# Kernel tuning notes

Hardware: AMD Instinct MI355X
Metric: run time of the kernel (lower is better)

The kernel has to match this reference:

```python
import jax, jax.numpy as jnp
import numpy as np

K_CLS, M_PROTO, C = 19, 10, 720
EPS_SK, SK_ITERS = 0.05, 3  # standard distributed_sinkhorn defaults (SwAV/ProtoSeg)


def _layernorm(x, g, b, eps=1e-5):
    mu = jnp.mean(x, axis=-1, keepdims=True)
    var = jnp.var(x, axis=-1, keepdims=True)
    return (x - mu) * jax.lax.rsqrt(var + eps) * g + b


def _l2n(x):
    return x / jnp.clip(jnp.linalg.norm(x, axis=-1, keepdims=True), 1e-12, None)


def _masked_sinkhorn(scores, mask):
    # scores: [K, N, M] per-class similarity; mask: [K, N] (1.0 where gt_seg == class k)
    # Faithful to distributed_sinkhorn(init_q) run per class, vectorized over classes
    # with masking instead of data-dependent boolean gather (jit-safe).
    L = jnp.exp(scores / EPS_SK) * mask[..., None]                     # [K, N, M]
    L = L / jnp.clip(jnp.sum(L, axis=(1, 2), keepdims=True), 1e-12, None)
    n = jnp.sum(mask, axis=1)[:, None, None]                           # pixels per class [K,1,1]
    n_safe = jnp.maximum(n, 1.0)

    def body(L, _):
        # normalize each prototype row (sum over pixels), then divide by M
        L = L / jnp.clip(jnp.sum(L, axis=1, keepdims=True), 1e-12, None) / M_PROTO
        # normalize each pixel column (sum over prototypes), then divide by n
        L = L / jnp.clip(jnp.sum(L, axis=2, keepdims=True), 1e-12, None) / n_safe
        L = L * mask[..., None]
        return L, None

    L, _ = jax.lax.scan(body, L, None, length=SK_ITERS)
    return L * n_safe                                                  # [K, N, M]


def setup_inputs() -> dict:
    key = jax.random.key(0)
    k1, k2, k3 = jax.random.split(key, 3)
    N = 4 * 128 * 128  # batch 4, 512x512 crop at HRNet output stride 4
    return {
        "x": jax.random.normal(k1, (N, C), jnp.float32),
        "gt_seg": jax.random.randint(k2, (N,), 0, K_CLS),
        "feat_gamma": jnp.ones((C,), jnp.float32),
        "feat_beta": jnp.zeros((C,), jnp.float32),
        "prototypes": jax.random.normal(k3, (K_CLS, M_PROTO, C), jnp.float32) * 0.02,
    }


def reference(x, gt_seg, feat_gamma, feat_beta, prototypes):
    # similarity_compute (cosine branch)
    xn = _l2n(_layernorm(x, feat_gamma, feat_beta))                    # [N, C]
    protos = _l2n(prototypes)                                          # [K, M, C]
    sim_mat = jnp.einsum('nd,kmd->nmk', xn, protos)                    # [N, M, K]

    # prototype_learning
    s = jnp.max(sim_mat, axis=1)                                       # amax over prototypes -> [N, K]
    pred_seg = jnp.argmax(s, axis=-1)                                  # [N]
    scores = jnp.transpose(sim_mat, (2, 0, 1))                         # [K, N, M]
    mask = jnp.transpose(jax.nn.one_hot(gt_seg, K_CLS, dtype=sim_mat.dtype))  # [K, N]
    q = _masked_sinkhorn(scores, mask)                                 # [K, N, M]
    return sim_mat, q, pred_seg
```

## Files before the change

### kernel.cpp

```cpp
#include <hip/hip_runtime.h>
#include <stdint.h>

#define N_PIX    65536
#define C_DIM    720
#define K_CLS    19
#define M_PROTO  10
#define NPROTO   190
#define CPAD     768
#define OFF_Q    12451840
#define OFF_PRED 24903680

typedef _Float16 half8 __attribute__((ext_vector_type(8)));
typedef float    f32x4 __attribute__((ext_vector_type(4)));

#define WS_E       0u
#define WS_G2      768u
#define WS_G3      1536u
#define WS_CNT     2304u
#define WS_TIECNT  2432u
#define WS_V       2560u
#define WS_PSCALE  4096u
#define WS_EPIX    1052672u
#define WS_U       3674112u
#define WS_TIELIST 3936256u
#define WS_PF16    4198400u
#define WS_PF32    4493312u

__global__ void zero_acc(float* ws) {
    if (threadIdx.x < 640) ws[threadIdx.x] = 0.f;
}

__global__ void proto_prep(const float* __restrict__ protos,
                           _Float16* __restrict__ pf16,
                           float* __restrict__ pf32) {
    int p = blockIdx.x;
    int tid = threadIdx.x;
    if (p >= NPROTO) {
        for (int c = tid; c < CPAD; c += 256) pf16[(size_t)p * CPAD + c] = (_Float16)0.f;
        return;
    }
    __shared__ float red[256];
    const float* row = protos + (size_t)p * C_DIM;
    float ss = 0.f;
    for (int c = tid; c < C_DIM; c += 256) { float v = row[c]; ss += v * v; }
    red[tid] = ss;
    __syncthreads();
    for (int s = 128; s > 0; s >>= 1) {
        if (tid < s) red[tid] += red[tid + s];
        __syncthreads();
    }
    float invn = 1.f / fmaxf(sqrtf(red[0]), 1e-12f);
    for (int c = tid; c < CPAD; c += 256) {
        float v = (c < C_DIM) ? row[c] * invn : 0.f;
        pf16[(size_t)p * CPAD + c] = (_Float16)v;
        if (c < C_DIM) pf32[(size_t)p * C_DIM + c] = v;
    }
}

__global__ void stats_kernel(const float* __restrict__ x,
                             const float* __restrict__ gamma,
                             const float* __restrict__ beta,
                             float4* __restrict__ pscale) {
    int wave = threadIdx.x >> 6, lane = threadIdx.x & 63;
    int n = blockIdx.x * 4 + wave;
    const float* row = x + (size_t)n * C_DIM;
    float a[8];
    #pragma unroll
    for (int t = 0; t < 8; ++t) a[t] = 0.f;
    #pragma unroll
    for (int j = 0; j < 12; ++j) {
        int i = lane + 64 * j;
        if (i < C_DIM) {
            float v = row[i], g = gamma[i], b = beta[i];
            float g2 = g * g;
            a[0] += v;          a[1] += v * v;
            a[2] += v * g2;     a[3] += v * v * g2;
            a[4] += v * g * b;  a[5] += g2;
            a[6] += g * b;      a[7] += b * b;
        }
    }
    #pragma unroll
    for (int m = 1; m < 64; m <<= 1) {
        #pragma unroll
        for (int t = 0; t < 8; ++t) a[t] += __shfl_xor(a[t], m);
    }
    if (lane == 0) {
        float mu   = a[0] * (1.f / 720.f);
        float var  = a[1] * (1.f / 720.f) - mu * mu;
        float rsig = rsqrtf(var + 1e-5f);
        float ny2  = rsig * rsig * (a[3] - 2.f * mu * a[2] + mu * mu * a[5])
                   + 2.f * rsig * (a[4] - mu * a[6]) + a[7];
        float rn   = 1.f / fmaxf(sqrtf(fmaxf(ny2, 0.f)), 1e-12f);
        float pp   = rsig * rn;
        pscale[n]  = make_float4(pp, -pp * mu, rn, 0.f);
    }
}

__global__ __launch_bounds__(256) void gemm_sim(
        const float*  __restrict__ x,
        const float4* __restrict__ pscale,
        const float*  __restrict__ gamma,
        const float*  __restrict__ beta,
        const _Float16* __restrict__ pf16,
        float* __restrict__ out) {
    __shared__ __align__(16) char smem[36864];
    _Float16* xs = (_Float16*)smem;
    _Float16* ps = (_Float16*)(smem + 9216);

    int tid = threadIdx.x;
    int wave = tid >> 6, lane = tid & 63;
    int lane15 = lane & 15, quad = lane >> 4;
    int n0 = blockIdx.x * 64;

    f32x4 acc[12];
    #pragma unroll
    for (int ct = 0; ct < 12; ++ct)
        acc[ct] = (f32x4){0.f, 0.f, 0.f, 0.f};

    #pragma unroll 1
    for (int ch = 0; ch < 12; ++ch) {
        __syncthreads();
        int kb4 = ch * 16;
        #pragma unroll
        for (int i = 0; i < 4; ++i) {
            int idx = tid + 256 * i;
            int r = idx >> 4, c4 = idx & 15;
            int gc4 = kb4 + c4;
            float4 xv = make_float4(0.f, 0.f, 0.f, 0.f);
            float4 gv = xv, bv = xv;
            if (gc4 < 180) {
                xv = *(const float4*)(x + (size_t)(n0 + r) * C_DIM + gc4 * 4);
                gv = *(const float4*)(gamma + gc4 * 4);
                bv = *(const float4*)(beta + gc4 * 4);
            }
            float4 sc = pscale[n0 + r];
            union { _Float16 h[4]; uint2 u; } cv;
            cv.h[0] = (_Float16)((sc.x * xv.x + sc.y) * gv.x + sc.z * bv.x);
            cv.h[1] = (_Float16)((sc.x * xv.y + sc.y) * gv.y + sc.z * bv.y);
            cv.h[2] = (_Float16)((sc.x * xv.z + sc.y) * gv.z + sc.z * bv.z);
            cv.h[3] = (_Float16)((sc.x * xv.w + sc.y) * gv.w + sc.z * bv.w);
            *reinterpret_cast<uint2*>(&xs[r * 72 + c4 * 4]) = cv.u;
        }
        #pragma unroll
        for (int i = 0; i < 6; ++i) {
            int idx = tid + 256 * i;
            int r = idx >> 3, c8 = idx & 7;
            int4 v = *(const int4*)(pf16 + (size_t)r * CPAD + ch * 64 + c8 * 8);
            *reinterpret_cast<int4*>(&ps[r * 72 + c8 * 8]) = v;
        }
        __syncthreads();
        #pragma unroll
        for (int ks = 0; ks < 2; ++ks) {
            int col = ks * 32 + quad * 8;
            half8 a0 = *reinterpret_cast<const half8*>(&xs[(wave * 16 + lane15) * 72 + col]);
            half8 b[12];
            #pragma unroll
            for (int ct = 0; ct < 12; ++ct)
                b[ct] = *reinterpret_cast<const half8*>(&ps[(ct * 16 + lane15) * 72 + col]);
            #pragma unroll
            for (int ct = 0; ct < 12; ++ct)
                acc[ct] = __builtin_amdgcn_mfma_f32_16x16x32_f16(a0, b[ct], acc[ct], 0, 0, 0);
        }
    }

    __syncthreads();
    float* ebuf = (float*)smem + wave * 1600;
    #pragma unroll
    for (int h = 0; h < 2; ++h) {
        if ((quad >> 1) == h) {
            int prow = (quad - 2 * h) * 4;
            #pragma unroll
            for (int ct = 0; ct < 12; ++ct) {
                int proto = ct * 16 + lane15;
                if (proto < NPROTO) {
                    int kc = proto / 10;
                    int m = proto - kc * 10;
                    int obase = m * 19 + kc;
                    #pragma unroll
                    for (int r = 0; r < 4; ++r)
                        ebuf[(prow + r) * 200 + obase] = acc[ct][r];
                }
            }
        }
        __syncthreads();
        #pragma unroll
        for (int p = 0; p < 8; ++p) {
            int pixel = n0 + wave * 16 + 8 * h + p;
            #pragma unroll
            for (int j = 0; j < 3; ++j) {
                int col = lane + 64 * j;
                if (col < NPROTO)
                    out[(size_t)pixel * 190 + col] = ebuf[p * 200 + col];
            }
        }
        __syncthreads();
    }
}

__global__ void reduce_pred(const float* __restrict__ sim,
                            const int* __restrict__ gt_seg,
                            float* __restrict__ out_pred,
                            float* __restrict__ epix,
                            float* __restrict__ E,
                            float* __restrict__ cnt,
                            int* __restrict__ tiecnt,
                            int* __restrict__ tielist) {
    __shared__ float Ek[192];
    __shared__ float hist[20];
    int tid = threadIdx.x;
    if (tid < 192) Ek[tid] = 0.f;
    if (tid < 20) hist[tid] = 0.f;
    __syncthreads();
    int n = blockIdx.x * 256 + tid;
    const float* row = sim + (size_t)n * 190;
    const float2* rp2 = reinterpret_cast<const float2*>(row);
    float s[19];
    #pragma unroll
    for (int k = 0; k < 19; ++k) s[k] = -1e30f;
    #pragma unroll
    for (int i = 0; i < 95; ++i) {
        float2 d = rp2[i];
        s[(2 * i) % 19]     = fmaxf(s[(2 * i) % 19], d.x);
        s[(2 * i + 1) % 19] = fmaxf(s[(2 * i + 1) % 19], d.y);
    }
    float best = s[0], second = -1e30f;
    int bk = 0;
    #pragma unroll
    for (int k = 1; k < 19; ++k) {
        float v = s[k];
        if (v > best) { second = best; best = v; bk = k; }
        else if (v > second) second = v;
    }
    out_pred[n] = (float)bk;
    if (best - second < 3e-4f) {
        int pos = atomicAdd(tiecnt, 1);
        if (pos < N_PIX) tielist[pos] = n;
    }
    int g = gt_seg[n];
    #pragma unroll
    for (int m = 0; m < 10; ++m) {
        float ev = __expf(row[m * 19 + g] * 20.f);
        epix[(size_t)n * 10 + m] = ev;
        atomicAdd(&Ek[g * 10 + m], ev);
    }
    atomicAdd(&hist[g], 1.f);
    __syncthreads();
    if (tid < 190) atomicAdd(&E[tid], Ek[tid]);
    if (tid < 19) atomicAdd(&cnt[tid], hist[tid]);
}

__global__ void tiefix(const float* __restrict__ x,
                       const float4* __restrict__ pscale,
                       const float* __restrict__ gamma,
                       const float* __restrict__ beta,
                       const float* __restrict__ pf32,
                       const int* __restrict__ tiecnt,
                       const int* __restrict__ tielist,
                       float* __restrict__ out_pred) {
    __shared__ float xrow[720];
    __shared__ double sd[190];
    int count = *tiecnt;
    if (count > N_PIX) count = N_PIX;
    int wave = threadIdx.x >> 6, lane = threadIdx.x & 63;
    for (int it = blockIdx.x; it < count; it += gridDim.x) {
        int n = tielist[it];
        float4 sc = pscale[n];
        for (int c = threadIdx.x; c < 720; c += 256)
            xrow[c] = (sc.x * x[(size_t)n * 720 + c] + sc.y) * gamma[c] + sc.z * beta[c];
        __syncthreads();
        for (int p = wave; p < NPROTO; p += 4) {
            const float* pr = pf32 + (size_t)p * 720;
            double a = 0.0;
            for (int j = 0; j < 12; ++j) {
                int i = lane + 64 * j;
                if (i < 720) a += (double)xrow[i] * (double)pr[i];
            }
            #pragma unroll
            for (int m = 1; m < 64; m <<= 1) a += __shfl_xor(a, m);
            if (lane == 0) sd[p] = a;
        }
        __syncthreads();
        if (threadIdx.x == 0) {
            double best = -1e300;
            int bk = 0;
            for (int k = 0; k < 19; ++k) {
                double sk = -1e300;
                for (int m = 0; m < 10; ++m) sk = fmax(sk, sd[k * 10 + m]);
                if (sk > best) { best = sk; bk = k; }
            }
            out_pred[n] = (float)bk;
        }
        __syncthreads();
    }
}

__global__ void v1k(const float* __restrict__ E, float* __restrict__ v) {
    __shared__ float Es[192];
    int t = threadIdx.x;
    if (t < 192) Es[t] = (t < 190) ? E[t] : 0.f;
    __syncthreads();
    if (t < 190) {
        int k = t / 10;
        float S = 0.f;
        #pragma unroll
        for (int m = 0; m < 10; ++m) S += Es[k * 10 + m];
        float v0 = 1.f / fmaxf(S, 1e-12f);
        float r = v0 * Es[t];
        v[t] = v0 / (fmaxf(r, 1e-12f) * 10.f);
    }
}

__global__ void v23k(float* __restrict__ v, const float* __restrict__ G) {
    int t = threadIdx.x;
    if (t < 190) {
        float r = v[t] * G[t];
        v[t] = v[t] / (fmaxf(r, 1e-12f) * 10.f);
    }
}

__global__ void pk(const float* __restrict__ epix,
                   const int* __restrict__ gt_seg,
                   const float* __restrict__ v,
                   const float* __restrict__ cnt,
                   const float* __restrict__ uin,
                   float* __restrict__ uout,
                   float* __restrict__ G) {
    __shared__ float vs[190];
    __shared__ float cs[19];
    __shared__ float Ga[190];
    int tid = threadIdx.x;
    if (tid < 190) { vs[tid] = v[tid]; Ga[tid] = 0.f; }
    if (tid < 19) cs[tid] = cnt[tid];
    __syncthreads();
    int n = blockIdx.x * 256 + tid;
    int g = gt_seg[n];
    float ns = fmaxf(cs[g], 1.f);
    const float* e = epix + (size_t)n * 10;
    float ev[10];
    float dot = 0.f;
    #pragma unroll
    for (int m = 0; m < 10; ++m) { ev[m] = e[m]; dot += ev[m] * vs[g * 10 + m]; }
    float up = uin ? uin[n] : 1.f;
    float c = up * dot;
    float u = up / (fmaxf(c, 1e-12f) * ns);
    uout[n] = u;
    #pragma unroll
    for (int m = 0; m < 10; ++m) atomicAdd(&Ga[g * 10 + m], ev[m] * u);
    __syncthreads();
    if (tid < 190) atomicAdd(&G[tid], Ga[tid]);
}

__global__ void p3k(const float* __restrict__ epix,
                    const int* __restrict__ gt_seg,
                    const float* __restrict__ v,
                    const float* __restrict__ cnt,
                    const float* __restrict__ uin,
                    float* __restrict__ qout) {
    __shared__ float vs[190];
    __shared__ float cs[19];
    int tid = threadIdx.x;
    if (tid < 190) vs[tid] = v[tid];
    if (tid < 19) cs[tid] = cnt[tid];
    __syncthreads();
    int n = blockIdx.x * 256 + tid;
    int g = gt_seg[n];
    float ns = fmaxf(cs[g], 1.f);
    const float* e = epix + (size_t)n * 10;
    float ev[10];
    float dot = 0.f;
    #pragma unroll
    for (int m = 0; m < 10; ++m) { ev[m] = e[m]; dot += ev[m] * vs[g * 10 + m]; }
    float up = uin[n];
    float c = up * dot;
    float u3 = up / (fmaxf(c, 1e-12f) * ns);
    float2 qv[5];
    #pragma unroll
    for (int j = 0; j < 5; ++j) {
        qv[j].x = ev[2 * j] * u3 * vs[g * 10 + 2 * j] * ns;
        qv[j].y = ev[2 * j + 1] * u3 * vs[g * 10 + 2 * j + 1] * ns;
    }
    const float2 z2 = make_float2(0.f, 0.f);
    for (int k = 0; k < 19; ++k) {
        float2* dst = reinterpret_cast<float2*>(qout + (size_t)k * 655360 + (size_t)n * 10);
        if (k == g) {
            #pragma unroll
            for (int j = 0; j < 5; ++j) dst[j] = qv[j];
        } else {
            #pragma unroll
            for (int j = 0; j < 5; ++j) dst[j] = z2;
        }
    }
}

extern "C" void kernel_launch(void* const* d_in, const int* in_sizes, int n_in,
                              void* d_out, int out_size, void* d_ws, size_t ws_size,
                              hipStream_t stream) {
    const float* x      = (const float*)d_in[0];
    const int*   gt     = (const int*)d_in[1];
    const float* gamma  = (const float*)d_in[2];
    const float* beta   = (const float*)d_in[3];
    const float* protos = (const float*)d_in[4];
    float* out = (float*)d_out;
    char* ws = (char*)d_ws;

    float*  E       = (float*)(ws + WS_E);
    float*  G2      = (float*)(ws + WS_G2);
    float*  G3      = (float*)(ws + WS_G3);
    float*  cnt     = (float*)(ws + WS_CNT);
    int*    tiecnt  = (int*)(ws + WS_TIECNT);
    float*  v       = (float*)(ws + WS_V);
    float4* pscale  = (float4*)(ws + WS_PSCALE);
    float*  epix    = (float*)(ws + WS_EPIX);
    float*  u       = (float*)(ws + WS_U);
    int*    tielist = (int*)(ws + WS_TIELIST);
    _Float16* pf16  = (_Float16*)(ws + WS_PF16);
    float*  pf32    = (float*)(ws + WS_PF32);

    zero_acc<<<1, 1024, 0, stream>>>((float*)ws);
    proto_prep<<<192, 256, 0, stream>>>(protos, pf16, pf32);
    stats_kernel<<<16384, 256, 0, stream>>>(x, gamma, beta, pscale);
    gemm_sim<<<1024, 256, 0, stream>>>(x, pscale, gamma, beta, pf16, out);
    reduce_pred<<<256, 256, 0, stream>>>(out, gt, out + OFF_PRED, epix, E, cnt, tiecnt, tielist);
    tiefix<<<1024, 256, 0, stream>>>(x, pscale, gamma, beta, pf32, tiecnt, tielist, out + OFF_PRED);
    v1k<<<1, 256, 0, stream>>>(E, v);
    pk<<<256, 256, 0, stream>>>(epix, gt, v, cnt, nullptr, u, G2);
    v23k<<<1, 256, 0, stream>>>(v, G2);
    pk<<<256, 256, 0, stream>>>(epix, gt, v, cnt, u, u, G3);
    v23k<<<1, 256, 0, stream>>>(v, G3);
    p3k<<<256, 256, 0, stream>>>(epix, gt, v, cnt, u, out + OFF_Q);
}
```

Before: 523.7 us.

## Fuse argmax, tie detection and exp/class sums into GEMM epilogue

Removes the separate reduce_pred kernel and computes per-pixel class maxima, argmax, tie listing, exp scores and per-class accumulations inside the gemm_sim epilogue from the LDS staging buffer. This avoids re-reading the 50MB similarity matrix from global memory and saves a launch. The trade-off is a longer epilogue that runs only 8 lanes per wave for the argmax and exp part, and extra barriers.

Measured after the change: 496.4 us. 5.2% less time.

```diff
diff --git a/kernel.cpp b/kernel.cpp
--- a/kernel.cpp
+++ b/kernel.cpp
@@ -102,7 +102,14 @@
         const float*  __restrict__ gamma,
         const float*  __restrict__ beta,
         const _Float16* __restrict__ pf16,
-        float* __restrict__ out) {
+        const int*    __restrict__ gt_seg,
+        float* __restrict__ out_sim,
+        float* __restrict__ out_pred,
+        float* __restrict__ epix,
+        float* __restrict__ E,
+        float* __restrict__ cnt,
+        int*   __restrict__ tiecnt,
+        int*   __restrict__ tielist) {
     __shared__ __align__(16) char smem[36864];
     _Float16* xs = (_Float16*)smem;
     _Float16* ps = (_Float16*)(smem + 9216);
@@ -164,7 +171,14 @@
     }
 
     __syncthreads();
-    float* ebuf = (float*)smem + wave * 1600;
+    float* fsm   = (float*)smem;
+    float* ebuf  = fsm + wave * 1600;
+    float* smaxw = fsm + 6400 + wave * 152;
+    float* Eks   = fsm + 7008;
+    float* hists = fsm + 7200;
+    if (tid < 212) fsm[7008 + tid] = 0.f;
+    __syncthreads();
+
     #pragma unroll
     for (int h = 0; h < 2; ++h) {
         if ((quad >> 1) == h) {
@@ -190,63 +204,49 @@
             for (int j = 0; j < 3; ++j) {
                 int col = lane + 64 * j;
                 if (col < NPROTO)
-                    out[(size_t)pixel * 190 + col] = ebuf[p * 200 + col];
-            }
-        }
-        __syncthreads();
-    }
-}
-
-__global__ void reduce_pred(const float* __restrict__ sim,
-                            const int* __restrict__ gt_seg,
-                            float* __restrict__ out_pred,
-                            float* __restrict__ epix,
-                            float* __restrict__ E,
-                            float* __restrict__ cnt,
-                            int* __restrict__ tiecnt,
-                            int* __restrict__ tielist) {
-    __shared__ float Ek[192];
-    __shared__ float hist[20];
-    int tid = threadIdx.x;
-    if (tid < 192) Ek[tid] = 0.f;
-    if (tid < 20) hist[tid] = 0.f;
-    __syncthreads();
-    int n = blockIdx.x * 256 + tid;
-    const float* row = sim + (size_t)n * 190;
-    const float2* rp2 = reinterpret_cast<const float2*>(row);
-    float s[19];
-    #pragma unroll
-    for (int k = 0; k < 19; ++k) s[k] = -1e30f;
-    #pragma unroll
-    for (int i = 0; i < 95; ++i) {
-        float2 d = rp2[i];
-        s[(2 * i) % 19]     = fmaxf(s[(2 * i) % 19], d.x);
-        s[(2 * i + 1) % 19] = fmaxf(s[(2 * i + 1) % 19], d.y);
-    }
-    float best = s[0], second = -1e30f;
-    int bk = 0;
-    #pragma unroll
-    for (int k = 1; k < 19; ++k) {
-        float v = s[k];
-        if (v > best) { second = best; best = v; bk = k; }
-        else if (v > second) second = v;
-    }
-    out_pred[n] = (float)bk;
-    if (best - second < 3e-4f) {
-        int pos = atomicAdd(tiecnt, 1);
-        if (pos < N_PIX) tielist[pos] = n;
-    }
-    int g = gt_seg[n];
-    #pragma unroll
-    for (int m = 0; m < 10; ++m) {
-        float ev = __expf(row[m * 19 + g] * 20.f);
-        epix[(size_t)n * 10 + m] = ev;
-        atomicAdd(&Ek[g * 10 + m], ev);
-    }
-    atomicAdd(&hist[g], 1.f);
-    __syncthreads();
-    if (tid < 190) atomicAdd(&E[tid], Ek[tid]);
-    if (tid < 19) atomicAdd(&cnt[tid], hist[tid]);
+                    out_sim[(size_t)pixel * 190 + col] = ebuf[p * 200 + col];
+            }
+        }
+        #pragma unroll
+        for (int t = lane; t < 152; t += 64) {
+            int p = t / 19, k = t - p * 19;
+            const float* row = ebuf + p * 200;
+            float mx = row[k];
+            #pragma unroll
+            for (int m = 1; m < 10; ++m) mx = fmaxf(mx, row[m * 19 + k]);
+            smaxw[t] = mx;
+        }
+        __syncthreads();
+        if (lane < 8) {
+            int p = lane;
+            int pixel = n0 + wave * 16 + 8 * h + p;
+            float best = smaxw[p * 19], second = -1e30f;
+            int bk = 0;
+            #pragma unroll
+            for (int k = 1; k < 19; ++k) {
+                float v = smaxw[p * 19 + k];
+                if (v > best) { second = best; best = v; bk = k; }
+                else if (v > second) second = v;
+            }
+            out_pred[pixel] = (float)bk;
+            if (best - second < 3e-4f) {
+                int pos = atomicAdd(tiecnt, 1);
+                if (pos < N_PIX) tielist[pos] = pixel;
+            }
+            int g = gt_seg[pixel];
+            atomicAdd(&hists[g], 1.f);
+            const float* row = ebuf + p * 200;
+            #pragma unroll
+            for (int m = 0; m < 10; ++m) {
+                float ev = __expf(row[m * 19 + g] * 20.f);
+                epix[(size_t)pixel * 10 + m] = ev;
+                atomicAdd(&Eks[g * 10 + m], ev);
+            }
+        }
+        __syncthreads();
+    }
+    if (tid < 190) atomicAdd(&E[tid], Eks[tid]);
+    if (tid < 19)  atomicAdd(&cnt[tid], hists[tid]);
 }
 
 __global__ void tiefix(const float* __restrict__ x,
@@ -419,8 +419,8 @@
     zero_acc<<<1, 1024, 0, stream>>>((float*)ws);
     proto_prep<<<192, 256, 0, stream>>>(protos, pf16, pf32);
     stats_kernel<<<16384, 256, 0, stream>>>(x, gamma, beta, pscale);
-    gemm_sim<<<1024, 256, 0, stream>>>(x, pscale, gamma, beta, pf16, out);
-    reduce_pred<<<256, 256, 0, stream>>>(out, gt, out + OFF_PRED, epix, E, cnt, tiecnt, tielist);
+    gemm_sim<<<1024, 256, 0, stream>>>(x, pscale, gamma, beta, pf16, gt,
+                                       out, out + OFF_PRED, epix, E, cnt, tiecnt, tielist);
     tiefix<<<1024, 256, 0, stream>>>(x, pscale, gamma, beta, pf32, tiecnt, tielist, out + OFF_PRED);
     v1k<<<1, 256, 0, stream>>>(E, v);
     pk<<<256, 256, 0, stream>>>(epix, gt, v, cnt, nullptr, u, G2);
```
